# Optimization experiments

Measured on AMD Instinct MI355X. Metric: run time of the kernel, lower is better.

The kernel has to match this reference:

```python
import jax, jax.numpy as jnp
import numpy as np

V, E, L, H = 128, 512, 8, 8
B, T = 4, 1024
EPS = 0.1  # label smoothing


def _ln(x, s, b):
    mu = x.mean(-1, keepdims=True)
    var = ((x - mu) ** 2).mean(-1, keepdims=True)
    return (x - mu) * jax.lax.rsqrt(var + 1e-5) * s + b


def _forward(inputs, targets, emb, qkv_w, qkv_b, aff1_w, aff1_b, aff2_w, aff2_b,
             ffn1_w, ffn1_b, ffn2_w, ffn2_b, ln1_s, ln1_b, ln2_s, ln2_b, head_w, head_b):
    Bx, Tx = inputs.shape
    x = emb[inputs]                                  # [B,T,E]
    dh = E // H
    mask = jnp.tril(jnp.ones((Tx, Tx), dtype=x.dtype))
    scale = np.float32(1.0 / np.sqrt(dh))
    for l in range(L):
        qkv = x @ qkv_w[l].T + qkv_b[l]              # [B,T,3E]
        qkv = qkv.reshape(Bx, Tx, H, 3 * dh).transpose(0, 2, 1, 3)  # [B,H,T,3dh]
        q, k, v = jnp.split(qkv, 3, axis=-1)
        # NOTE: original multiplies scores by boolean tril mask (zeros, not -inf)
        scores = jnp.einsum('bhqd,bhkd->bhqk', q, k) * mask * scale
        att = jax.nn.softmax(scores, axis=-1) @ v    # [B,H,T,dh]
        att = att.transpose(0, 2, 1, 3).reshape(Bx, Tx, E)
        att = jax.nn.relu(att @ aff1_w[l].T + aff1_b[l]) @ aff2_w[l].T + aff2_b[l]
        out1 = _ln(att + x, ln1_s[l], ln1_b[l])
        out2 = jax.nn.relu(out1 @ ffn1_w[l].T + ffn1_b[l]) @ ffn2_w[l].T + ffn2_b[l]
        x = _ln(out1 + out2, ln2_s[l], ln2_b[l])
    logits = x @ head_w.T + head_b                   # [B,T,V]
    logp = jax.nn.log_softmax(logits, axis=-1)
    nll = -jnp.take_along_axis(logp, targets[..., None], axis=-1)[..., 0]
    smooth = -logp.mean(-1)
    loss = jnp.mean((1.0 - EPS) * nll + EPS * smooth)
    return logits, loss


def setup_inputs() -> dict:
    key = jax.random.key(0)
    ks = jax.random.split(key, 16)
    s = lambda k, shape, fan: (jax.random.normal(k, shape, jnp.float32) / np.sqrt(fan)).astype(jnp.float32)
    return {
        'inputs': jax.random.randint(ks[0], (B, T), 0, V, dtype=jnp.int32).astype(jnp.int64),
        'targets': jax.random.randint(ks[1], (B, T), 0, V, dtype=jnp.int32).astype(jnp.int64),
        'emb': s(ks[2], (V, E), 1.0),
        'qkv_w': s(ks[3], (L, 3 * E, E), E),
        'qkv_b': jnp.zeros((L, 3 * E), jnp.float32),
        'aff1_w': s(ks[4], (L, E, E), E),
        'aff1_b': jnp.zeros((L, E), jnp.float32),
        'aff2_w': s(ks[5], (L, E, E), E),
        'aff2_b': jnp.zeros((L, E), jnp.float32),
        'ffn1_w': s(ks[6], (L, E, E), E),
        'ffn1_b': jnp.zeros((L, E), jnp.float32),
        'ffn2_w': s(ks[7], (L, E, E), E),
        'ffn2_b': jnp.zeros((L, E), jnp.float32),
        'ln1_s': jnp.ones((L, E), jnp.float32),
        'ln1_b': jnp.zeros((L, E), jnp.float32),
        'ln2_s': jnp.ones((L, E), jnp.float32),
        'ln2_b': jnp.zeros((L, E), jnp.float32),
        'head_w': s(ks[8], (V, E), E),
        'head_b': jnp.zeros((V,), jnp.float32),
    }


def reference(inputs, targets, emb, qkv_w, qkv_b, aff1_w, aff1_b, aff2_w, aff2_b,
              ffn1_w, ffn1_b, ffn2_w, ffn2_b, ln1_s, ln1_b, ln2_s, ln2_b, head_w, head_b):
    return _forward(inputs, targets, emb, qkv_w, qkv_b, aff1_w, aff1_b, aff2_w, aff2_b,
                    ffn1_w, ffn1_b, ffn2_w, ffn2_b, ln1_s, ln1_b, ln2_s, ln2_b, head_w, head_b)
```

## Files before the change

kernel.cpp:

```cpp
#include <hip/hip_runtime.h>


#define V_  128
#define E_  512
#define L_  8
#define H_  8
#define B_  4
#define T_  1024
#define N_  (B_*T_)
#define DH_ 64
#define E3_ 1536

typedef __attribute__((ext_vector_type(8))) short   bf16x8;
typedef __attribute__((ext_vector_type(4))) float   floatx4;

#define SW(row,k8) (((row) << 6) + ((((k8) ^ ((row) & 7))) << 3))

__device__ __forceinline__ unsigned short f2bf(float f) {
    union { float f; unsigned int i; } v; v.f = f;
    unsigned int x = v.i;
    return (unsigned short)((x + 0x7fffu + ((x >> 16) & 1u)) >> 16);
}
__device__ __forceinline__ float bf2f(unsigned short u) {
    union { unsigned int i; float f; } v; v.i = ((unsigned int)u) << 16; return v.f;
}
__device__ __forceinline__ void gload_lds16(const void* g, void* l) {
    __builtin_amdgcn_global_load_lds(
        (const __attribute__((address_space(1))) unsigned int*)g,
        (__attribute__((address_space(3))) unsigned int*)l, 16, 0, 0);
}

__device__ __forceinline__ void xcd_remap(int& mstrip, int& nblk) {
    int nx = gridDim.x;
    int flat = blockIdx.y * nx + blockIdx.x;
    int xcd = flat & 7;
    int j = flat >> 3;
    int per_xcd = gridDim.y >> 3;
    mstrip = xcd * per_xcd + j / nx;
    nblk = j % nx;
}

#define CVT_N0 6291456
#define CVT_N1 2097152
#define CVT_TOT (CVT_N0 + 4*CVT_N1 + V_*E_)
__global__ void cvt_all_kernel(const float* __restrict__ s0, const float* __restrict__ s1,
                               const float* __restrict__ s2, const float* __restrict__ s3,
                               const float* __restrict__ s4, const float* __restrict__ s5,
                               unsigned short* __restrict__ dst) {
    long i = (long)(blockIdx.x * blockDim.x + threadIdx.x) * 4;
    if (i >= CVT_TOT) return;
    const float* src; long off;
    if      (i < CVT_N0)               { src = s0; off = i; }
    else if (i < CVT_N0 + CVT_N1)      { src = s1; off = i - CVT_N0; }
    else if (i < CVT_N0 + 2*CVT_N1)    { src = s2; off = i - CVT_N0 - CVT_N1; }
    else if (i < CVT_N0 + 3*CVT_N1)    { src = s3; off = i - CVT_N0 - 2L*CVT_N1; }
    else if (i < CVT_N0 + 4*CVT_N1)    { src = s4; off = i - CVT_N0 - 3L*CVT_N1; }
    else                               { src = s5; off = i - CVT_N0 - 4L*CVT_N1; }
    float4 v = *(const float4*)(src + off);
    ushort4 o; o.x = f2bf(v.x); o.y = f2bf(v.y); o.z = f2bf(v.z); o.w = f2bf(v.w);
    *(ushort4*)(dst + i) = o;
}

__global__ void embed_kernel(const int* __restrict__ tok, const float* __restrict__ emb,
                             float* __restrict__ xf, unsigned short* __restrict__ xb) {
    int idx = blockIdx.x * blockDim.x + threadIdx.x;
    if (idx >= N_ * E_) return;
    int n = idx >> 9;
    int e = idx & (E_ - 1);
    float v = emb[tok[n] * E_ + e];
    xf[idx] = v; xb[idx] = f2bf(v);
}

template<int RELU, int WF, int WB>
__global__ __launch_bounds__(256) void gemm64(
    const unsigned short* __restrict__ A, const unsigned short* __restrict__ W,
    const float* __restrict__ bias, float* __restrict__ Cf, unsigned short* __restrict__ Cb,
    int M, int Nout, int K)
{
    __shared__ unsigned short Asm[4][64 * 64];
    __shared__ unsigned short Bsm[4][64 * 64];
    int tid = threadIdx.x;
    int wv = tid >> 6, ln = tid & 63;
    int lquad = ln >> 4, lmod = ln & 15;
    int mstrip, nblk;
    xcd_remap(mstrip, nblk);
    int m0 = mstrip * 64, n0 = nblk * 64;

    floatx4 acc[4] = {};

    auto stage = [&](int k0, int s) {
        #pragma unroll
        for (int c = 0; c < 2; ++c) {
            int cc = tid + 256 * c;
            int r = cc >> 3, k8s = (cc & 7) ^ (r & 7);
            gload_lds16(A + (size_t)(m0 + r) * K + k0 + 8 * k8s,
                        &Asm[s][2048 * c + 512 * wv]);
        }
        #pragma unroll
        for (int c = 0; c < 2; ++c) {
            int cc = tid + 256 * c;
            int r = cc >> 3, k8s = (cc & 7) ^ (r & 7);
            gload_lds16(W + (size_t)(n0 + r) * K + k0 + 8 * k8s,
                        &Bsm[s][2048 * c + 512 * wv]);
        }
    };

    int np = K >> 7;
    stage(0, 0);
    stage(64, 1);
    __syncthreads();

    for (int t = 0; t < np; ++t) {
        if (t + 1 < np) {
            stage((2 * t + 2) << 6, (2 * t + 2) & 3);
            stage((2 * t + 3) << 6, (2 * t + 3) & 3);
        }
        #pragma unroll
        for (int half = 0; half < 2; ++half) {
            int s = (2 * t + half) & 3;
            #pragma unroll
            for (int ks = 0; ks < 2; ++ks) {
                bf16x8 af = *(const bf16x8*)&Asm[s][SW(16 * wv + lmod, ks * 4 + lquad)];
                #pragma unroll
                for (int j = 0; j < 4; ++j) {
                    bf16x8 bfr = *(const bf16x8*)&Bsm[s][SW(16 * j + lmod, ks * 4 + lquad)];
                    acc[j] = __builtin_amdgcn_mfma_f32_16x16x32_bf16(af, bfr, acc[j], 0, 0, 0);
                }
            }
        }
        if (t + 1 < np) __syncthreads();
    }

    #pragma unroll
    for (int j = 0; j < 4; ++j) {
        int n = n0 + 16 * j + lmod;
        float bj = bias[n];
        #pragma unroll
        for (int v = 0; v < 4; ++v) {
            int m = m0 + 16 * wv + 4 * lquad + v;
            float val = acc[j][v] + bj;
            if (RELU) val = fmaxf(val, 0.f);
            if (WF) Cf[(size_t)m * Nout + n] = val;
            if (WB) Cb[(size_t)m * Nout + n] = f2bf(val);
        }
    }
}

__global__ __launch_bounds__(256) void gemm_qkv(
    const unsigned short* __restrict__ A, const unsigned short* __restrict__ W,
    const float* __restrict__ bias, unsigned short* __restrict__ Cb,
    unsigned short* __restrict__ vt_g, float* __restrict__ vtile, int K)
{
    __shared__ unsigned short Asm[2][128 * 64];
    __shared__ unsigned short Bsm[2][64 * 64];
    __shared__ float vred[4][64];
    int tid = threadIdx.x;
    int wv = tid >> 6, ln = tid & 63;
    int lquad = ln >> 4, lmod = ln & 15;
    int mstrip, nblk;
    xcd_remap(mstrip, nblk);
    int m0 = mstrip * 128, n0 = nblk * 64;

    floatx4 acc[2][4] = {};

    auto stage = [&](int k0, int pb) {
        #pragma unroll
        for (int c = 0; c < 4; ++c) {
            int cc = tid + 256 * c;
            int r = cc >> 3, k8s = (cc & 7) ^ (r & 7);
            gload_lds16(A + (size_t)(m0 + r) * K + k0 + 8 * k8s,
                        &Asm[pb][2048 * c + 512 * wv]);
        }
        #pragma unroll
        for (int c = 0; c < 2; ++c) {
            int cc = tid + 256 * c;
            int r = cc >> 3, k8s = (cc & 7) ^ (r & 7);
            gload_lds16(W + (size_t)(n0 + r) * K + k0 + 8 * k8s,
                        &Bsm[pb][2048 * c + 512 * wv]);
        }
    };

    int nt = K >> 6;
    stage(0, 0);
    __syncthreads();
    for (int t = 0; t < nt; ++t) {
        int pb = t & 1;
        if (t + 1 < nt) stage((t + 1) << 6, pb ^ 1);
        #pragma unroll
        for (int ks = 0; ks < 2; ++ks) {
            bf16x8 af[2], bfr[4];
            #pragma unroll
            for (int i = 0; i < 2; ++i)
                af[i] = *(const bf16x8*)&Asm[pb][SW(32 * wv + 16 * i + lmod, ks * 4 + lquad)];
            #pragma unroll
            for (int j = 0; j < 4; ++j)
                bfr[j] = *(const bf16x8*)&Bsm[pb][SW(16 * j + lmod, ks * 4 + lquad)];
            #pragma unroll
            for (int i = 0; i < 2; ++i)
                #pragma unroll
                for (int j = 0; j < 4; ++j)
                    acc[i][j] = __builtin_amdgcn_mfma_f32_16x16x32_bf16(af[i], bfr[j], acc[i][j], 0, 0, 0);
        }
        if (t + 1 < nt) __syncthreads();
    }

    if ((n0 % 192) != 128) {
        #pragma unroll
        for (int i = 0; i < 2; ++i)
            #pragma unroll
            for (int j = 0; j < 4; ++j) {
                int n = n0 + 16 * j + lmod;
                float bj = bias[n];
                #pragma unroll
                for (int v = 0; v < 4; ++v) {
                    int m = m0 + 32 * wv + 16 * i + 4 * lquad + v;
                    Cb[(size_t)m * E3_ + n] = f2bf(acc[i][j][v] + bj);
                }
            }
    } else {
        int h = n0 / 192;
        int b = m0 >> 10;
        int bh = b * 8 + h;
        int t0 = m0 & 1023;
        int kt0 = t0 >> 6;
        float sj[4] = {0.f, 0.f, 0.f, 0.f};
        #pragma unroll
        for (int j = 0; j < 4; ++j) {
            float bj = bias[n0 + 16 * j + lmod];
            #pragma unroll
            for (int i = 0; i < 2; ++i) {
                union { unsigned short u[4]; uint2 q; } pk;
                #pragma unroll
                for (int v = 0; v < 4; ++v) {
                    unsigned short r = f2bf(acc[i][j][v] + bj);
                    pk.u[v] = r;
                    sj[j] += bf2f(r);
                }
                int t = t0 + 32 * wv + 16 * i + 4 * lquad;
                *(uint2*)&vt_g[((size_t)(bh * 64 + 16 * j + lmod)) * T_ + t] = pk.q;
            }
        }
        #pragma unroll
        for (int j = 0; j < 4; ++j) {
            sj[j] += __shfl_xor(sj[j], 16);
            sj[j] += __shfl_xor(sj[j], 32);
        }
        if (lquad == 0) {
            #pragma unroll
            for (int j = 0; j < 4; ++j) vred[wv][16 * j + lmod] = sj[j];
        }
        __syncthreads();
        if (tid < 128) {
            int half = tid >> 6, d = tid & 63;
            vtile[((size_t)bh * 16 + kt0 + half) * 64 + d] =
                vred[2 * half][d] + vred[2 * half + 1][d];
        }
    }
}

__global__ __launch_bounds__(256) void attn_mfma(const unsigned short* __restrict__ qkv,
                                                 const unsigned short* __restrict__ vt_g,
                                                 const float* __restrict__ vtile,
                                                 unsigned short* __restrict__ outb)
{
    __shared__ unsigned short Qs[64 * 64];
    __shared__ unsigned short Ks[2][64 * 64];
    __shared__ unsigned short Vs[2][64 * 64];
    __shared__ unsigned short Ps[64 * 64];

    int tid = threadIdx.x;
    int wv = tid >> 6, ln = tid & 63;
    int lquad = ln >> 4, lmod = ln & 15;
    int bh = blockIdx.x;
    int y = blockIdx.y;
    int qt = (y < 8) ? y : 23 - y;
    int b = bh >> 3, h = bh & 7;
    int q0 = qt * 64;
    const float scale = 0.125f;
    size_t base = (size_t)b * T_ * E3_ + h * 192;

    auto stageKV = [&](int k0, int pb) {
        #pragma unroll
        for (int c = 0; c < 2; ++c) {
            int cc = tid + 256 * c;
            int r = cc >> 3, k8s = (cc & 7) ^ (r & 7);
            gload_lds16(qkv + base + (size_t)(k0 + r) * E3_ + 64 + 8 * k8s,
                        &Ks[pb][2048 * c + 512 * wv]);
            gload_lds16(vt_g + ((size_t)(bh * 64 + r)) * T_ + k0 + 8 * k8s,
                        &Vs[pb][2048 * c + 512 * wv]);
        }
    };

    #pragma unroll
    for (int c = 0; c < 2; ++c) {
        int cc = tid + 256 * c;
        int r = cc >> 3, k8s = (cc & 7) ^ (r & 7);
        gload_lds16(qkv + base + (size_t)(q0 + r) * E3_ + 8 * k8s, Qs + 2048 * c + 512 * wv);
    }
    stageKV(0, 0);
    __syncthreads();

    float lrow[4] = {0.f, 0.f, 0.f, 0.f};
    floatx4 Oa[4] = {};

    for (int kt = 0; kt <= qt; ++kt) {
        int pb = kt & 1;
        int k0 = kt * 64;
        if (kt < qt) stageKV(k0 + 64, pb ^ 1);

        floatx4 sacc[4] = {};
        #pragma unroll
        for (int ks = 0; ks < 2; ++ks) {
            bf16x8 aq = *(const bf16x8*)&Qs[SW(16 * wv + lmod, ks * 4 + lquad)];
            #pragma unroll
            for (int j = 0; j < 4; ++j) {
                bf16x8 bk = *(const bf16x8*)&Ks[pb][SW(16 * j + lmod, ks * 4 + lquad)];
                sacc[j] = __builtin_amdgcn_mfma_f32_16x16x32_bf16(aq, bk, sacc[j], 0, 0, 0);
            }
        }
        #pragma unroll
        for (int v = 0; v < 4; ++v) {
            int qg = q0 + 16 * wv + 4 * lquad + v;
            int row = 16 * wv + 4 * lquad + v;
            #pragma unroll
            for (int j = 0; j < 4; ++j) {
                int kg = k0 + 16 * j + lmod;
                float p = (kg <= qg) ? __expf(sacc[j][v] * scale) : 1.0f;
                lrow[v] += p;
                int col = 16 * j + lmod;
                Ps[SW(row, col >> 3) + (col & 7)] = f2bf(p);
            }
        }
        asm volatile("s_waitcnt lgkmcnt(0)" ::: "memory");
        __builtin_amdgcn_sched_barrier(0);

        #pragma unroll
        for (int ks = 0; ks < 2; ++ks) {
            bf16x8 ap = *(const bf16x8*)&Ps[SW(16 * wv + lmod, ks * 4 + lquad)];
            #pragma unroll
            for (int f = 0; f < 4; ++f) {
                bf16x8 bv = *(const bf16x8*)&Vs[pb][SW(16 * f + lmod, ks * 4 + lquad)];
                Oa[f] = __builtin_amdgcn_mfma_f32_16x16x32_bf16(ap, bv, Oa[f], 0, 0, 0);
            }
        }
        if (kt < qt) __syncthreads();
    }

    #pragma unroll
    for (int v = 0; v < 4; ++v)
        #pragma unroll
        for (int msk = 1; msk < 16; msk <<= 1) lrow[v] += __shfl_xor(lrow[v], msk);

    if (qt < 15) {
        float Km = (float)((15 - qt) * 64);
        #pragma unroll
        for (int v = 0; v < 4; ++v) lrow[v] += Km;
        #pragma unroll
        for (int f = 0; f < 4; ++f) {
            float sv = 0.f;
            for (int kt = qt + 1; kt < 16; ++kt)
                sv += vtile[((size_t)bh * 16 + kt) * 64 + 16 * f + lmod];
            #pragma unroll
            for (int v = 0; v < 4; ++v) Oa[f][v] += sv;
        }
    }

    #pragma unroll
    for (int f = 0; f < 4; ++f)
        #pragma unroll
        for (int v = 0; v < 4; ++v) {
            int q = q0 + 16 * wv + 4 * lquad + v;
            outb[(size_t)(b * T_ + q) * E_ + h * DH_ + 16 * f + lmod] = f2bf(Oa[f][v] / lrow[v]);
        }
}

__global__ __launch_bounds__(256) void add_ln_kernel(
    const float* __restrict__ a, const float* __restrict__ r,
    const float* __restrict__ s, const float* __restrict__ bpar,
    float* __restrict__ outF, unsigned short* __restrict__ outB)
{
    int tid = threadIdx.x, wv = tid >> 6, ln = tid & 63;
    int n = blockIdx.x * 4 + wv;
    int e = ln * 8;
    size_t base = (size_t)n * E_ + e;
    float4 a0 = *(const float4*)&a[base],     a1 = *(const float4*)&a[base + 4];
    float4 r0 = *(const float4*)&r[base],     r1 = *(const float4*)&r[base + 4];
    float v[8] = {a0.x + r0.x, a0.y + r0.y, a0.z + r0.z, a0.w + r0.w,
                  a1.x + r1.x, a1.y + r1.y, a1.z + r1.z, a1.w + r1.w};

    float sm = 0.f;
    #pragma unroll
    for (int i = 0; i < 8; ++i) sm += v[i];
    #pragma unroll
    for (int msk = 1; msk < 64; msk <<= 1) sm += __shfl_xor(sm, msk);
    float mu = sm * (1.f / 512.f);

    float ss = 0.f;
    #pragma unroll
    for (int i = 0; i < 8; ++i) { v[i] -= mu; ss += v[i] * v[i]; }
    #pragma unroll
    for (int msk = 1; msk < 64; msk <<= 1) ss += __shfl_xor(ss, msk);
    float rstd = rsqrtf(ss * (1.f / 512.f) + 1e-5f);

    float4 sc0 = *(const float4*)&s[e],    sc1 = *(const float4*)&s[e + 4];
    float4 bp0 = *(const float4*)&bpar[e], bp1 = *(const float4*)&bpar[e + 4];
    float o[8];
    o[0] = v[0] * rstd * sc0.x + bp0.x; o[1] = v[1] * rstd * sc0.y + bp0.y;
    o[2] = v[2] * rstd * sc0.z + bp0.z; o[3] = v[3] * rstd * sc0.w + bp0.w;
    o[4] = v[4] * rstd * sc1.x + bp1.x; o[5] = v[5] * rstd * sc1.y + bp1.y;
    o[6] = v[6] * rstd * sc1.z + bp1.z; o[7] = v[7] * rstd * sc1.w + bp1.w;
    *(float4*)&outF[base]     = make_float4(o[0], o[1], o[2], o[3]);
    *(float4*)&outF[base + 4] = make_float4(o[4], o[5], o[6], o[7]);
    union { unsigned short u[8]; uint4 q; } pk;
    #pragma unroll
    for (int i = 0; i < 8; ++i) pk.u[i] = f2bf(o[i]);
    *(uint4*)&outB[base] = pk.q;
}

__global__ __launch_bounds__(256) void head_loss_kernel(
    const unsigned short* __restrict__ A, const unsigned short* __restrict__ W,
    const float* __restrict__ bias, const int* __restrict__ tgt,
    float* __restrict__ out_logits, float* __restrict__ rowloss)
{
    __shared__ unsigned short Asm[2][64 * 64];
    __shared__ unsigned short Bsm[2][128 * 64];
    int tid = threadIdx.x;
    int wv = tid >> 6, ln = tid & 63;
    int lquad = ln >> 4, lmod = ln & 15;
    int m0 = blockIdx.x * 64;

    floatx4 acc[8] = {};

    auto stage = [&](int k0, int pb) {
        #pragma unroll
        for (int c = 0; c < 2; ++c) {
            int cc = tid + 256 * c;
            int r = cc >> 3, k8s = (cc & 7) ^ (r & 7);
            gload_lds16(A + (size_t)(m0 + r) * E_ + k0 + 8 * k8s,
                        &Asm[pb][2048 * c + 512 * wv]);
        }
        #pragma unroll
        for (int c = 0; c < 4; ++c) {
            int cc = tid + 256 * c;
            int r = cc >> 3, k8s = (cc & 7) ^ (r & 7);
            gload_lds16(W + (size_t)r * E_ + k0 + 8 * k8s,
                        &Bsm[pb][2048 * c + 512 * wv]);
        }
    };

    stage(0, 0);
    __syncthreads();
    for (int t = 0; t < 8; ++t) {
        int pb = t & 1;
        if (t < 7) stage((t + 1) << 6, pb ^ 1);
        #pragma unroll
        for (int ks = 0; ks < 2; ++ks) {
            bf16x8 af = *(const bf16x8*)&Asm[pb][SW(16 * wv + lmod, ks * 4 + lquad)];
            #pragma unroll
            for (int j = 0; j < 8; ++j) {
                bf16x8 bf = *(const bf16x8*)&Bsm[pb][SW(16 * j + lmod, ks * 4 + lquad)];
                acc[j] = __builtin_amdgcn_mfma_f32_16x16x32_bf16(af, bf, acc[j], 0, 0, 0);
            }
        }
        if (t < 7) __syncthreads();
    }

    float bj[8];
    #pragma unroll
    for (int j = 0; j < 8; ++j) bj[j] = bias[16 * j + lmod];
    #pragma unroll
    for (int v = 0; v < 4; ++v) {
        int m = m0 + 16 * wv + 4 * lquad + v;
        float x[8];
        float mx = -1e30f, sx = 0.f;
        #pragma unroll
        for (int j = 0; j < 8; ++j) {
            x[j] = acc[j][v] + bj[j];
            out_logits[(size_t)m * V_ + 16 * j + lmod] = x[j];
            mx = fmaxf(mx, x[j]); sx += x[j];
        }
        #pragma unroll
        for (int msk = 1; msk < 16; msk <<= 1) mx = fmaxf(mx, __shfl_xor(mx, msk));
        float se = 0.f;
        #pragma unroll
        for (int j = 0; j < 8; ++j) se += __expf(x[j] - mx);
        #pragma unroll
        for (int msk = 1; msk < 16; msk <<= 1) {
            se += __shfl_xor(se, msk);
            sx += __shfl_xor(sx, msk);
        }
        int t = tgt[m];
        float cand = 0.f;
        #pragma unroll
        for (int j = 0; j < 8; ++j) cand = ((t >> 4) == j) ? x[j] : cand;
        float xt = __shfl(cand, (ln & 48) | (t & 15));
        if (lmod == 0) {
            float lse = mx + __logf(se);
            rowloss[m] = 0.9f * (lse - xt) + 0.1f * (lse - sx * (1.f / 128.f));
        }
    }
}

__global__ __launch_bounds__(256) void loss_reduce_kernel(
    const float* __restrict__ rowloss, float* __restrict__ out)
{
    int tid = threadIdx.x;
    float sm = 0.f;
    for (int idx = tid; idx < N_; idx += 256) sm += rowloss[idx];
    #pragma unroll
    for (int off = 32; off; off >>= 1) sm += __shfl_down(sm, off, 64);
    __shared__ float red[4];
    int lane = tid & 63, w = tid >> 6;
    if (lane == 0) red[w] = sm;
    __syncthreads();
    if (tid == 0) out[0] = (red[0] + red[1] + red[2] + red[3]) * (1.f / (float)N_);
}

extern "C" void kernel_launch(void* const* d_in, const int* in_sizes, int n_in,
                              void* d_out, int out_size, void* d_ws, size_t ws_size,
                              hipStream_t stream)
{
    (void)in_sizes; (void)n_in; (void)out_size; (void)ws_size;
    const int* toks     = (const int*)d_in[0];
    const int* tgts     = (const int*)d_in[1];
    const float* emb    = (const float*)d_in[2];
    const float* qkv_w  = (const float*)d_in[3];
    const float* qkv_b  = (const float*)d_in[4];
    const float* aff1_w = (const float*)d_in[5];
    const float* aff1_b = (const float*)d_in[6];
    const float* aff2_w = (const float*)d_in[7];
    const float* aff2_b = (const float*)d_in[8];
    const float* ffn1_w = (const float*)d_in[9];
    const float* ffn1_b = (const float*)d_in[10];
    const float* ffn2_w = (const float*)d_in[11];
    const float* ffn2_b = (const float*)d_in[12];
    const float* ln1_s  = (const float*)d_in[13];
    const float* ln1_b  = (const float*)d_in[14];
    const float* ln2_s  = (const float*)d_in[15];
    const float* ln2_b  = (const float*)d_in[16];
    const float* head_w = (const float*)d_in[17];
    const float* head_b = (const float*)d_in[18];

    char* p = (char*)d_ws;
    auto carve = [&](size_t bytes) { char* r = p; p += (bytes + 255) & ~(size_t)255; return (void*)r; };
    unsigned short* wb_all  = (unsigned short*)carve((size_t)CVT_TOT * 2);
    unsigned short* wb_qkv  = wb_all;
    unsigned short* wb_aff1 = wb_qkv  + (size_t)CVT_N0;
    unsigned short* wb_aff2 = wb_aff1 + (size_t)CVT_N1;
    unsigned short* wb_ffn1 = wb_aff2 + (size_t)CVT_N1;
    unsigned short* wb_ffn2 = wb_ffn1 + (size_t)CVT_N1;
    unsigned short* wb_head = wb_ffn2 + (size_t)CVT_N1;
    float*          x_f     = (float*)carve((size_t)N_ * E_ * 4);
    unsigned short* x_b     = (unsigned short*)carve((size_t)N_ * E_ * 2);
    unsigned short* qkv_bf  = (unsigned short*)carve((size_t)N_ * E3_ * 2);
    unsigned short* att_b   = (unsigned short*)carve((size_t)N_ * E_ * 2);
    unsigned short* h_b     = (unsigned short*)carve((size_t)N_ * E_ * 2);
    float*          y_f     = (float*)carve((size_t)N_ * E_ * 4);
    float*          o1_f    = (float*)carve((size_t)N_ * E_ * 4);
    unsigned short* o1_b    = (unsigned short*)carve((size_t)N_ * E_ * 2);
    float*          rowl    = (float*)carve((size_t)N_ * 4);
    float*          vtile   = (float*)carve((size_t)32 * 16 * 64 * 4);
    unsigned short* vt_g    = (unsigned short*)carve((size_t)32 * 64 * T_ * 2);

    float* out_logits = (float*)d_out;
    float* out_loss   = out_logits + (size_t)N_ * V_;

    cvt_all_kernel<<<dim3(CVT_TOT / 1024), 256, 0, stream>>>(
        qkv_w, aff1_w, aff2_w, ffn1_w, ffn2_w, head_w, wb_all);

    embed_kernel<<<dim3((N_ * E_) / 256), 256, 0, stream>>>(toks, emb, x_f, x_b);

    for (int l = 0; l < L_; ++l) {
        gemm_qkv<<<dim3(E3_/64, N_/128), 256, 0, stream>>>(
            x_b, wb_qkv + (size_t)l * E3_ * E_, qkv_b + (size_t)l * E3_,
            qkv_bf, vt_g, vtile, E_);
        attn_mfma<<<dim3(32, 16), 256, 0, stream>>>(qkv_bf, vt_g, vtile, att_b);
        gemm64<1,0,1><<<dim3(E_/64, N_/64), 256, 0, stream>>>(
            att_b, wb_aff1 + (size_t)l * E_ * E_, aff1_b + (size_t)l * E_,
            nullptr, h_b, N_, E_, E_);
        gemm64<0,1,0><<<dim3(E_/64, N_/64), 256, 0, stream>>>(
            h_b, wb_aff2 + (size_t)l * E_ * E_, aff2_b + (size_t)l * E_,
            y_f, nullptr, N_, E_, E_);
        add_ln_kernel<<<dim3(N_/4), 256, 0, stream>>>(
            y_f, x_f, ln1_s + (size_t)l * E_, ln1_b + (size_t)l * E_, o1_f, o1_b);
        gemm64<1,0,1><<<dim3(E_/64, N_/64), 256, 0, stream>>>(
            o1_b, wb_ffn1 + (size_t)l * E_ * E_, ffn1_b + (size_t)l * E_,
            nullptr, h_b, N_, E_, E_);
        gemm64<0,1,0><<<dim3(E_/64, N_/64), 256, 0, stream>>>(
            h_b, wb_ffn2 + (size_t)l * E_ * E_, ffn2_b + (size_t)l * E_,
            y_f, nullptr, N_, E_, E_);
        add_ln_kernel<<<dim3(N_/4), 256, 0, stream>>>(
            o1_f, y_f, ln2_s + (size_t)l * E_, ln2_b + (size_t)l * E_, x_f, x_b);
    }

    head_loss_kernel<<<dim3(N_/64), 256, 0, stream>>>(
        x_b, wb_head, head_b, tgts, out_logits, rowl);
    loss_reduce_kernel<<<dim3(1), 256, 0, stream>>>(rowl, out_loss);
}
```

Baseline: 796.8 us.

## Use triple-buffered LDS pipelines with partial vmcnt waits in GEMM and attention

Both the generic GEMM and the attention kernel move to a three-stage ring buffer that prefetches two tiles ahead. Each stage waits with a partial vmcnt and a raw s_barrier instead of a full __syncthreads drain, so the next tile's global-to-LDS loads can stay in flight during compute. The GEMM drops from four to three LDS buffers and now syncs once per 64-wide K step instead of once per 128. Attention grows from two to three K/V buffers. The partial-wait counts rely on each stage issuing exactly four loads per thread, and raising LDS use in attention may lower occupancy.

```diff
diff --git a/kernel.cpp b/kernel.cpp
--- a/kernel.cpp
+++ b/kernel.cpp
@@ -15,6 +15,9 @@
 typedef __attribute__((ext_vector_type(4))) float   floatx4;
 
 #define SW(row,k8) (((row) << 6) + ((((k8) ^ ((row) & 7))) << 3))
+
+#define WAIT_VM4 asm volatile("s_waitcnt vmcnt(4)" ::: "memory")
+#define WAIT_VM0 asm volatile("s_waitcnt vmcnt(0)" ::: "memory")
 
 __device__ __forceinline__ unsigned short f2bf(float f) {
     union { float f; unsigned int i; } v; v.f = f;
@@ -77,8 +80,8 @@
     const float* __restrict__ bias, float* __restrict__ Cf, unsigned short* __restrict__ Cb,
     int M, int Nout, int K)
 {
-    __shared__ unsigned short Asm[4][64 * 64];
-    __shared__ unsigned short Bsm[4][64 * 64];
+    __shared__ unsigned short Asm[3][64 * 64];
+    __shared__ unsigned short Bsm[3][64 * 64];
     int tid = threadIdx.x;
     int wv = tid >> 6, ln = tid & 63;
     int lquad = ln >> 4, lmod = ln & 15;
@@ -105,30 +108,30 @@
         }
     };
 
-    int np = K >> 7;
+    int nt = K >> 6;
     stage(0, 0);
     stage(64, 1);
-    __syncthreads();
-
-    for (int t = 0; t < np; ++t) {
-        if (t + 1 < np) {
-            stage((2 * t + 2) << 6, (2 * t + 2) & 3);
-            stage((2 * t + 3) << 6, (2 * t + 3) & 3);
-        }
-        #pragma unroll
-        for (int half = 0; half < 2; ++half) {
-            int s = (2 * t + half) & 3;
-            #pragma unroll
-            for (int ks = 0; ks < 2; ++ks) {
-                bf16x8 af = *(const bf16x8*)&Asm[s][SW(16 * wv + lmod, ks * 4 + lquad)];
-                #pragma unroll
-                for (int j = 0; j < 4; ++j) {
-                    bf16x8 bfr = *(const bf16x8*)&Bsm[s][SW(16 * j + lmod, ks * 4 + lquad)];
-                    acc[j] = __builtin_amdgcn_mfma_f32_16x16x32_bf16(af, bfr, acc[j], 0, 0, 0);
-                }
+    WAIT_VM4;
+    __builtin_amdgcn_s_barrier();
+    __builtin_amdgcn_sched_barrier(0);
+
+    for (int t = 0; t < nt; ++t) {
+        int s = t % 3;
+        if (t + 2 < nt) stage((t + 2) << 6, (t + 2) % 3);
+        #pragma unroll
+        for (int ks = 0; ks < 2; ++ks) {
+            bf16x8 af = *(const bf16x8*)&Asm[s][SW(16 * wv + lmod, ks * 4 + lquad)];
+            #pragma unroll
+            for (int j = 0; j < 4; ++j) {
+                bf16x8 bfr = *(const bf16x8*)&Bsm[s][SW(16 * j + lmod, ks * 4 + lquad)];
+                acc[j] = __builtin_amdgcn_mfma_f32_16x16x32_bf16(af, bfr, acc[j], 0, 0, 0);
             }
         }
-        if (t + 1 < np) __syncthreads();
+        if (t + 1 < nt) {
+            if (t + 2 < nt) WAIT_VM4; else WAIT_VM0;
+            __builtin_amdgcn_s_barrier();
+            __builtin_amdgcn_sched_barrier(0);
+        }
     }
 
     #pragma unroll
@@ -264,8 +267,8 @@
                                                  unsigned short* __restrict__ outb)
 {
     __shared__ unsigned short Qs[64 * 64];
-    __shared__ unsigned short Ks[2][64 * 64];
-    __shared__ unsigned short Vs[2][64 * 64];
+    __shared__ unsigned short Ks[3][64 * 64];
+    __shared__ unsigned short Vs[3][64 * 64];
     __shared__ unsigned short Ps[64 * 64];
 
     int tid = threadIdx.x;
@@ -279,15 +282,15 @@
     const float scale = 0.125f;
     size_t base = (size_t)b * T_ * E3_ + h * 192;
 
-    auto stageKV = [&](int k0, int pb) {
+    auto stageKV = [&](int k0, int s) {
         #pragma unroll
         for (int c = 0; c < 2; ++c) {
             int cc = tid + 256 * c;
             int r = cc >> 3, k8s = (cc & 7) ^ (r & 7);
             gload_lds16(qkv + base + (size_t)(k0 + r) * E3_ + 64 + 8 * k8s,
-                        &Ks[pb][2048 * c + 512 * wv]);
+                        &Ks[s][2048 * c + 512 * wv]);
             gload_lds16(vt_g + ((size_t)(bh * 64 + r)) * T_ + k0 + 8 * k8s,
-                        &Vs[pb][2048 * c + 512 * wv]);
+                        &Vs[s][2048 * c + 512 * wv]);
         }
     };
 
@@ -298,15 +301,22 @@
         gload_lds16(qkv + base + (size_t)(q0 + r) * E3_ + 8 * k8s, Qs + 2048 * c + 512 * wv);
     }
     stageKV(0, 0);
-    __syncthreads();
+    if (qt >= 1) {
+        stageKV(64, 1);
+        WAIT_VM4;
+    } else {
+        WAIT_VM0;
+    }
+    __builtin_amdgcn_s_barrier();
+    __builtin_amdgcn_sched_barrier(0);
 
     float lrow[4] = {0.f, 0.f, 0.f, 0.f};
     floatx4 Oa[4] = {};
 
     for (int kt = 0; kt <= qt; ++kt) {
-        int pb = kt & 1;
+        int s = kt % 3;
         int k0 = kt * 64;
-        if (kt < qt) stageKV(k0 + 64, pb ^ 1);
+        if (kt + 2 <= qt) stageKV(k0 + 128, (kt + 2) % 3);
 
         floatx4 sacc[4] = {};
         #pragma unroll
@@ -314,7 +324,7 @@
             bf16x8 aq = *(const bf16x8*)&Qs[SW(16 * wv + lmod, ks * 4 + lquad)];
             #pragma unroll
             for (int j = 0; j < 4; ++j) {
-                bf16x8 bk = *(const bf16x8*)&Ks[pb][SW(16 * j + lmod, ks * 4 + lquad)];
+                bf16x8 bk = *(const bf16x8*)&Ks[s][SW(16 * j + lmod, ks * 4 + lquad)];
                 sacc[j] = __builtin_amdgcn_mfma_f32_16x16x32_bf16(aq, bk, sacc[j], 0, 0, 0);
             }
         }
@@ -339,11 +349,15 @@
             bf16x8 ap = *(const bf16x8*)&Ps[SW(16 * wv + lmod, ks * 4 + lquad)];
             #pragma unroll
             for (int f = 0; f < 4; ++f) {
-                bf16x8 bv = *(const bf16x8*)&Vs[pb][SW(16 * f + lmod, ks * 4 + lquad)];
+                bf16x8 bv = *(const bf16x8*)&Vs[s][SW(16 * f + lmod, ks * 4 + lquad)];
                 Oa[f] = __builtin_amdgcn_mfma_f32_16x16x32_bf16(ap, bv, Oa[f], 0, 0, 0);
             }
         }
-        if (kt < qt) __syncthreads();
+        if (kt < qt) {
+            if (kt + 2 <= qt) WAIT_VM4; else WAIT_VM0;
+            __builtin_amdgcn_s_barrier();
+            __builtin_amdgcn_sched_barrier(0);
+        }
     }
 
     #pragma unroll
```

After: 825.2 us. 3.6% more time.

## Split GEMM K across wave pairs and fuse residual add into epilogue

Applied to the files above, without the earlier changes.

The 64x64 GEMM now gives each wave a 32x64 sub-tile over half of each K chunk, instead of a 16x64 strip over the full chunk. This reuses each loaded B fragment across two A fragments, cutting LDS reads per MFMA. The two K-halves are reduced through shared memory in the epilogue, which adds a barrier and an LDS round-trip. Separately, the residual add moves into the aff2/ffn2 GEMM epilogue, so the LayerNorm kernel reads one fp32 tensor instead of two.

```diff
diff --git a/kernel.cpp b/kernel.cpp
--- a/kernel.cpp
+++ b/kernel.cpp
@@ -71,10 +71,11 @@
     xf[idx] = v; xb[idx] = f2bf(v);
 }
 
-template<int RELU, int WF, int WB>
+template<int RELU, int WF, int WB, int ADDRES>
 __global__ __launch_bounds__(256) void gemm64(
     const unsigned short* __restrict__ A, const unsigned short* __restrict__ W,
-    const float* __restrict__ bias, float* __restrict__ Cf, unsigned short* __restrict__ Cb,
+    const float* __restrict__ bias, const float* __restrict__ resF,
+    float* __restrict__ Cf, unsigned short* __restrict__ Cb,
     int M, int Nout, int K)
 {
     __shared__ unsigned short Asm[4][64 * 64];
@@ -82,11 +83,12 @@
     int tid = threadIdx.x;
     int wv = tid >> 6, ln = tid & 63;
     int lquad = ln >> 4, lmod = ln & 15;
+    int mh = wv & 1, kh = wv >> 1;
     int mstrip, nblk;
     xcd_remap(mstrip, nblk);
     int m0 = mstrip * 64, n0 = nblk * 64;
 
-    floatx4 acc[4] = {};
+    floatx4 acc[2][4] = {};
 
     auto stage = [&](int k0, int s) {
         #pragma unroll
@@ -118,31 +120,52 @@
         #pragma unroll
         for (int half = 0; half < 2; ++half) {
             int s = (2 * t + half) & 3;
-            #pragma unroll
-            for (int ks = 0; ks < 2; ++ks) {
-                bf16x8 af = *(const bf16x8*)&Asm[s][SW(16 * wv + lmod, ks * 4 + lquad)];
+            bf16x8 af[2], bfr[4];
+            #pragma unroll
+            for (int i = 0; i < 2; ++i)
+                af[i] = *(const bf16x8*)&Asm[s][SW(32 * mh + 16 * i + lmod, 4 * kh + lquad)];
+            #pragma unroll
+            for (int j = 0; j < 4; ++j)
+                bfr[j] = *(const bf16x8*)&Bsm[s][SW(16 * j + lmod, 4 * kh + lquad)];
+            #pragma unroll
+            for (int i = 0; i < 2; ++i)
                 #pragma unroll
-                for (int j = 0; j < 4; ++j) {
-                    bf16x8 bfr = *(const bf16x8*)&Bsm[s][SW(16 * j + lmod, ks * 4 + lquad)];
-                    acc[j] = __builtin_amdgcn_mfma_f32_16x16x32_bf16(af, bfr, acc[j], 0, 0, 0);
+                for (int j = 0; j < 4; ++j)
+                    acc[i][j] = __builtin_amdgcn_mfma_f32_16x16x32_bf16(af[i], bfr[j], acc[i][j], 0, 0, 0);
+        }
+        if (t + 1 < np) __syncthreads();
+    }
+
+    float* redF = (float*)&Asm[0][0];
+    if (kh == 1) {
+        #pragma unroll
+        for (int i = 0; i < 2; ++i)
+            #pragma unroll
+            for (int j = 0; j < 4; ++j) {
+                int bidx = i * 4 + j;
+                *(floatx4*)&redF[mh * 2048 + ln * 32 + (((bidx ^ (ln & 7))) << 2)] = acc[i][j];
+            }
+    }
+    __syncthreads();
+    if (kh == 0) {
+        #pragma unroll
+        for (int i = 0; i < 2; ++i)
+            #pragma unroll
+            for (int j = 0; j < 4; ++j) {
+                int bidx = i * 4 + j;
+                floatx4 part = *(const floatx4*)&redF[mh * 2048 + ln * 32 + (((bidx ^ (ln & 7))) << 2)];
+                int n = n0 + 16 * j + lmod;
+                float bj = bias[n];
+                #pragma unroll
+                for (int v = 0; v < 4; ++v) {
+                    int m = m0 + 32 * mh + 16 * i + 4 * lquad + v;
+                    float val = acc[i][j][v] + part[v] + bj;
+                    if (ADDRES) val += resF[(size_t)m * Nout + n];
+                    if (RELU) val = fmaxf(val, 0.f);
+                    if (WF) Cf[(size_t)m * Nout + n] = val;
+                    if (WB) Cb[(size_t)m * Nout + n] = f2bf(val);
                 }
             }
-        }
-        if (t + 1 < np) __syncthreads();
-    }
-
-    #pragma unroll
-    for (int j = 0; j < 4; ++j) {
-        int n = n0 + 16 * j + lmod;
-        float bj = bias[n];
-        #pragma unroll
-        for (int v = 0; v < 4; ++v) {
-            int m = m0 + 16 * wv + 4 * lquad + v;
-            float val = acc[j][v] + bj;
-            if (RELU) val = fmaxf(val, 0.f);
-            if (WF) Cf[(size_t)m * Nout + n] = val;
-            if (WB) Cb[(size_t)m * Nout + n] = f2bf(val);
-        }
     }
 }
 
@@ -374,8 +397,8 @@
         }
 }
 
-__global__ __launch_bounds__(256) void add_ln_kernel(
-    const float* __restrict__ a, const float* __restrict__ r,
+__global__ __launch_bounds__(256) void ln_kernel(
+    const float* __restrict__ z,
     const float* __restrict__ s, const float* __restrict__ bpar,
     float* __restrict__ outF, unsigned short* __restrict__ outB)
 {
@@ -383,10 +406,8 @@
     int n = blockIdx.x * 4 + wv;
     int e = ln * 8;
     size_t base = (size_t)n * E_ + e;
-    float4 a0 = *(const float4*)&a[base],     a1 = *(const float4*)&a[base + 4];
-    float4 r0 = *(const float4*)&r[base],     r1 = *(const float4*)&r[base + 4];
-    float v[8] = {a0.x + r0.x, a0.y + r0.y, a0.z + r0.z, a0.w + r0.w,
-                  a1.x + r1.x, a1.y + r1.y, a1.z + r1.z, a1.w + r1.w};
+    float4 a0 = *(const float4*)&z[base], a1 = *(const float4*)&z[base + 4];
+    float v[8] = {a0.x, a0.y, a0.z, a0.w, a1.x, a1.y, a1.z, a1.w};
 
     float sm = 0.f;
     #pragma unroll
@@ -575,22 +596,22 @@
             x_b, wb_qkv + (size_t)l * E3_ * E_, qkv_b + (size_t)l * E3_,
             qkv_bf, vt_g, vtile, E_);
         attn_mfma<<<dim3(32, 16), 256, 0, stream>>>(qkv_bf, vt_g, vtile, att_b);
-        gemm64<1,0,1><<<dim3(E_/64, N_/64), 256, 0, stream>>>(
+        gemm64<1,0,1,0><<<dim3(E_/64, N_/64), 256, 0, stream>>>(
             att_b, wb_aff1 + (size_t)l * E_ * E_, aff1_b + (size_t)l * E_,
-            nullptr, h_b, N_, E_, E_);
-        gemm64<0,1,0><<<dim3(E_/64, N_/64), 256, 0, stream>>>(
+            nullptr, nullptr, h_b, N_, E_, E_);
+        gemm64<0,1,0,1><<<dim3(E_/64, N_/64), 256, 0, stream>>>(
             h_b, wb_aff2 + (size_t)l * E_ * E_, aff2_b + (size_t)l * E_,
-            y_f, nullptr, N_, E_, E_);
-        add_ln_kernel<<<dim3(N_/4), 256, 0, stream>>>(
-            y_f, x_f, ln1_s + (size_t)l * E_, ln1_b + (size_t)l * E_, o1_f, o1_b);
-        gemm64<1,0,1><<<dim3(E_/64, N_/64), 256, 0, stream>>>(
+            x_f, y_f, nullptr, N_, E_, E_);
+        ln_kernel<<<dim3(N_/4), 256, 0, stream>>>(
+            y_f, ln1_s + (size_t)l * E_, ln1_b + (size_t)l * E_, o1_f, o1_b);
+        gemm64<1,0,1,0><<<dim3(E_/64, N_/64), 256, 0, stream>>>(
             o1_b, wb_ffn1 + (size_t)l * E_ * E_, ffn1_b + (size_t)l * E_,
-            nullptr, h_b, N_, E_, E_);
-        gemm64<0,1,0><<<dim3(E_/64, N_/64), 256, 0, stream>>>(
+            nullptr, nullptr, h_b, N_, E_, E_);
+        gemm64<0,1,0,1><<<dim3(E_/64, N_/64), 256, 0, stream>>>(
             h_b, wb_ffn2 + (size_t)l * E_ * E_, ffn2_b + (size_t)l * E_,
-            y_f, nullptr, N_, E_, E_);
-        add_ln_kernel<<<dim3(N_/4), 256, 0, stream>>>(
-            o1_f, y_f, ln2_s + (size_t)l * E_, ln2_b + (size_t)l * E_, x_f, x_b);
+            o1_f, y_f, nullptr, N_, E_, E_);
+        ln_kernel<<<dim3(N_/4), 256, 0, stream>>>(
+            y_f, ln2_s + (size_t)l * E_, ln2_b + (size_t)l * E_, x_f, x_b);
     }
 
     head_loss_kernel<<<dim3(N_/64), 256, 0, stream>>>(
```

Result: faster. 780.6 us (-2.0%).
